# Kernel optimization log

Hardware: AMD Instinct MI355X
Metric: run time of the kernel (lower is better)

## Reference

```python
import jax, jax.numpy as jnp
import numpy as np

N = 100000   # nodes
E = 1600000  # edges
DIN, H, DOUT = 128, 64, 40
EPS = 1e-5

def setup_inputs() -> dict:
    key = jax.random.key(0)
    ks = jax.random.split(key, 8)
    def w(k, fan_in, shape):
        return jax.random.normal(k, shape, jnp.float32) * (1.0 / np.sqrt(fan_in))
    return {
        "node_feat": jax.random.normal(ks[0], (N, DIN), jnp.float32),
        "edge_index": jax.random.randint(ks[1], (2, E), 0, N, dtype=jnp.int32),
        "W1": w(ks[2], DIN, (DIN, H)), "b1": jnp.zeros((H,), jnp.float32),
        "g1": jnp.ones((H,), jnp.float32), "beta1": jnp.zeros((H,), jnp.float32),
        "W2": w(ks[3], H, (H, H)), "b2": jnp.zeros((H,), jnp.float32),
        "g2": jnp.ones((H,), jnp.float32), "beta2": jnp.zeros((H,), jnp.float32),
        "W3": w(ks[4], H, (H, H)), "b3": jnp.zeros((H,), jnp.float32),
        "Wf": w(ks[5], H, (H, DOUT)), "bf": jnp.zeros((DOUT,), jnp.float32),
    }

def _gcn_conv(x, src, dst, norm, W, b):
    # x: [N, Cin] -> linear then D^{-1/2}(A+I)D^{-1/2} aggregation (PyG GCNConv)
    h = x @ W                              # [N, Cout]
    msg = h[src] * norm[:, None]           # [E+N, Cout] gather + scale
    return jax.ops.segment_sum(msg, dst, num_segments=N) + b

def _bn(x, g, b):
    # BatchNorm1d over node dim with batch statistics (biased var)
    m = jnp.mean(x, axis=0)
    v = jnp.mean((x - m) ** 2, axis=0)
    return (x - m) * jax.lax.rsqrt(v + EPS) * g + b

def reference(node_feat, edge_index, W1, b1, g1, beta1, W2, b2, g2, beta2, W3, b3, Wf, bf):
    loop = jnp.arange(N, dtype=edge_index.dtype)
    src = jnp.concatenate([edge_index[0], loop])   # add self loops
    dst = jnp.concatenate([edge_index[1], loop])
    deg = jax.ops.segment_sum(jnp.ones_like(src, dtype=node_feat.dtype), dst, num_segments=N)
    dis = jax.lax.rsqrt(deg)                        # deg >= 1 (self loops)
    norm = dis[src] * dis[dst]                      # [E+N]

    x1 = jax.nn.relu(_bn(_gcn_conv(node_feat, src, dst, norm, W1, b1), g1, beta1))
    # dropout is identity in eval mode
    x2 = jax.nn.relu(_bn(_gcn_conv(x1, src, dst, norm, W2, b2), g2, beta2))
    x3 = _gcn_conv(x2, src, dst, norm, W3, b3)

    x = jnp.max(jnp.stack([x1, x2, x3], axis=0), axis=0)  # JumpingKnowledge 'max'
    return x @ Wf + bf
```

## Files before the change

### kernel.cpp

```cpp
#include <hip/hip_runtime.h>

#define NN 100000
#define NE 1600000
#define DIN 128
#define HDIM 64
#define DOUT 40
#define EPS 1e-5f
#define NXCD 8
#define CAP 64

typedef int int4v __attribute__((ext_vector_type(4)));
typedef float f4v __attribute__((ext_vector_type(4)));

__device__ __forceinline__ float bf2f(unsigned short v) {
    return __uint_as_float(((unsigned int)v) << 16);
}
__device__ __forceinline__ unsigned short f2bf(float f) {
    unsigned int u = __float_as_uint(f);
    u += 0x7FFFu + ((u >> 16) & 1u);
    return (unsigned short)(u >> 16);
}

__device__ __forceinline__ int ntl(const int* p) { return __builtin_nontemporal_load(p); }
__device__ __forceinline__ int4v ntl4(const int4v* p) { return __builtin_nontemporal_load(p); }
__device__ __forceinline__ f4v ntlf4(const f4v* p) { return __builtin_nontemporal_load(p); }

__global__ __launch_bounds__(256) void fill_kernel(const int* __restrict__ ei,
                                                   int* __restrict__ cnt,
                                                   int* __restrict__ esrc) {
    const int xcd = blockIdx.x & (NXCD - 1);
    const int lo = xcd * (NN / NXCD);
    const int hi = (xcd == NXCD - 1) ? NN : lo + (NN / NXCD);
    const int slot = blockIdx.x >> 3;
    const int nslot = gridDim.x >> 3;
    const int4v* d4 = (const int4v*)(ei + NE);
    for (int e4 = slot * blockDim.x + threadIdx.x; e4 < NE / 4; e4 += nslot * blockDim.x) {
        int4v d = ntl4(d4 + e4);
#pragma unroll
        for (int k = 0; k < 4; ++k) {
            int dd = d[k];
            if (dd >= lo && dd < hi) {
                int pos = atomicAdd(&cnt[dd], 1);
                if (pos < CAP) {
                    esrc[(dd << 6) + pos] = ntl(ei + 4 * e4 + k);
                }
            }
        }
    }
}

__global__ __launch_bounds__(256) void dis_kernel(const int* __restrict__ cnt,
                                                  float* __restrict__ dis) {
    for (int i = blockIdx.x * blockDim.x + threadIdx.x; i < NN; i += gridDim.x * blockDim.x)
        dis[i] = rsqrtf((float)(cnt[i] + 1));
}

template <int K, int TR, bool BN, bool NTL>
__global__ __launch_bounds__(256) void gemm_lds(const float* __restrict__ x,
                                                const float* __restrict__ W,
                                                const float* __restrict__ dis,
                                                const float* __restrict__ sc,
                                                const float* __restrict__ sh,
                                                unsigned short* __restrict__ h2) {
    __shared__ float xs[TR][K];
    const int tid = threadIdx.x;
    const int lane = tid & 63;
    const int wv = tid >> 6;
    float w[K];
#pragma unroll
    for (int k = 0; k < K; ++k) w[k] = W[k * 64 + lane];

    float4 scv, shv;
    if (BN) {
        const int c4 = tid & (K / 4 - 1);
        scv = ((const float4*)sc)[c4];
        shv = ((const float4*)sh)[c4];
    }

    const int row0 = blockIdx.x * TR;
    const int remRows = NN - row0;
    const int nvec = ((remRows >= TR) ? TR : remRows) * K / 4;
    const f4v* srcv = (const f4v*)(x + (long long)row0 * K);
    f4v* dstv = (f4v*)&xs[0][0];
    for (int i = tid; i < nvec; i += 256) {
        f4v v = NTL ? ntlf4(srcv + i) : srcv[i];
        if (BN) {
            v.x = fmaxf(fmaf(v.x, scv.x, shv.x), 0.f);
            v.y = fmaxf(fmaf(v.y, scv.y, shv.y), 0.f);
            v.z = fmaxf(fmaf(v.z, scv.z, shv.z), 0.f);
            v.w = fmaxf(fmaf(v.w, scv.w, shv.w), 0.f);
        }
        dstv[i] = v;
    }
    __syncthreads();

    const int rpw = TR / 4;
#pragma unroll
    for (int rr = 0; rr < rpw; ++rr) {
        const int r = wv * rpw + rr;
        const int row = row0 + r;
        if (row >= NN) break;
        float a0 = 0.f, a1 = 0.f, a2 = 0.f, a3 = 0.f;
#pragma unroll
        for (int k = 0; k < K; k += 4) {
            float4 xv = *(const float4*)&xs[r][k];
            a0 = fmaf(xv.x, w[k + 0], a0);
            a1 = fmaf(xv.y, w[k + 1], a1);
            a2 = fmaf(xv.z, w[k + 2], a2);
            a3 = fmaf(xv.w, w[k + 3], a3);
        }
        h2[row * 64 + lane] = f2bf(((a0 + a1) + (a2 + a3)) * dis[row]);
    }
}

__global__ __launch_bounds__(256) void agg_csr(const int* __restrict__ cnt,
                                               const int* __restrict__ esrc,
                                               const float* __restrict__ dis,
                                               const unsigned short* __restrict__ h2,
                                               float* __restrict__ y) {
    const int tid = threadIdx.x;
    const int wv = tid >> 6;
    const int lane = tid & 63;
    const int half = lane >> 5;
    const int c = lane & 31;
    const int node = blockIdx.x * 8 + wv * 2 + half;
    const ushort2* h2v = (const ushort2*)h2;
    ushort2 p0 = h2v[node * 32 + c];
    float ax = bf2f(p0.x), ay = bf2f(p0.y);
    const int deg = min(cnt[node], CAP);
    const int m = max(deg, __shfl_xor(deg, 32));
    const int jb = node << 6;
#pragma unroll 8
    for (int t = 0; t < m; ++t) {
        int sv = esrc[jb + t];
        int s = (t < deg) ? sv : NN;
        ushort2 p = h2v[s * 32 + c];
        ax += bf2f(p.x);
        ay += bf2f(p.y);
    }
    float dn = dis[node];
    ((float2*)(y + node * 64))[c] = make_float2(ax * dn, ay * dn);
}

__global__ __launch_bounds__(256) void agg_final(const int* __restrict__ cnt,
                                                 const int* __restrict__ esrc,
                                                 const float* __restrict__ dis,
                                                 const unsigned short* __restrict__ h2,
                                                 const float* __restrict__ x1,
                                                 const float* __restrict__ x2,
                                                 const float* __restrict__ sc1,
                                                 const float* __restrict__ sh1,
                                                 const float* __restrict__ sc2,
                                                 const float* __restrict__ sh2,
                                                 const float* __restrict__ b3,
                                                 const float* __restrict__ Wf,
                                                 const float* __restrict__ bf,
                                                 float* __restrict__ out) {
    __shared__ float m[8][64];
    const int tid = threadIdx.x;
    const int wv = tid >> 6;
    const int lane = tid & 63;
    const int half = lane >> 5;
    const int c = lane & 31;
    const int node = blockIdx.x * 8 + wv * 2 + half;
    const ushort2* h2v = (const ushort2*)h2;
    ushort2 p0 = h2v[node * 32 + c];
    float ax = bf2f(p0.x), ay = bf2f(p0.y);
    const int deg = min(cnt[node], CAP);
    const int mm = max(deg, __shfl_xor(deg, 32));
    const int jb = node << 6;
#pragma unroll 8
    for (int t = 0; t < mm; ++t) {
        int sv = esrc[jb + t];
        int s = (t < deg) ? sv : NN;
        ushort2 p = h2v[s * 32 + c];
        ax += bf2f(p.x);
        ay += bf2f(p.y);
    }
    const float dn = dis[node];
    const int c0 = 2 * c;
    const int o = node * 64 + c0;
    float2 x1v = *(const float2*)(x1 + o);
    float2 x2v = *(const float2*)(x2 + o);
    float v3x = fmaf(ax, dn, b3[c0]);
    float v3y = fmaf(ay, dn, b3[c0 + 1]);
    float v1x = fmaxf(fmaf(x1v.x, sc1[c0], sh1[c0]), 0.f);
    float v1y = fmaxf(fmaf(x1v.y, sc1[c0 + 1], sh1[c0 + 1]), 0.f);
    float v2x = fmaxf(fmaf(x2v.x, sc2[c0], sh2[c0]), 0.f);
    float v2y = fmaxf(fmaf(x2v.y, sc2[c0 + 1], sh2[c0 + 1]), 0.f);
    const int rl = wv * 2 + half;
    m[rl][c0] = fmaxf(fmaxf(v1x, v2x), v3x);
    m[rl][c0 + 1] = fmaxf(fmaxf(v1y, v2y), v3y);
    __syncthreads();
#pragma unroll
    for (int rr = wv; rr < 8; rr += 4) {
        if (lane < DOUT) {
            float a2 = bf[lane];
#pragma unroll
            for (int k = 0; k < 64; ++k) a2 += m[rr][k] * Wf[k * DOUT + lane];
            out[(blockIdx.x * 8 + rr) * DOUT + lane] = a2;
        }
    }
}

__global__ __launch_bounds__(256) void stats_kernel(const float* __restrict__ y, float* stats) {
    const int tid = threadIdx.x;
    const int c = tid & 63, rg = tid >> 6;
    float s = 0.f, s2 = 0.f;
    for (int row = blockIdx.x * 4 + rg; row < NN; row += gridDim.x * 4) {
        float v = y[row * 64 + c];
        s += v;
        s2 += v * v;
    }
    __shared__ float ls[256], ls2[256];
    ls[tid] = s; ls2[tid] = s2;
    __syncthreads();
    if (tid < 64) {
        s = ls[tid] + ls[tid + 64] + ls[tid + 128] + ls[tid + 192];
        s2 = ls2[tid] + ls2[tid + 64] + ls2[tid + 128] + ls2[tid + 192];
        atomicAdd(&stats[tid], s);
        atomicAdd(&stats[64 + tid], s2);
    }
}

__global__ __launch_bounds__(64) void bn_coef(const float* __restrict__ stats,
                                              const float* __restrict__ g,
                                              const float* __restrict__ beta,
                                              float* __restrict__ sc,
                                              float* __restrict__ sh) {
    const int c = threadIdx.x;
    const float invN = 1.0f / NN;
    float m = stats[c] * invN;
    float var = stats[64 + c] * invN - m * m;
    float s = g[c] * rsqrtf(var + EPS);
    sc[c] = s;
    sh[c] = beta[c] - m * s;
}

extern "C" void kernel_launch(void* const* d_in, const int* in_sizes, int n_in,
                              void* d_out, int out_size, void* d_ws, size_t ws_size,
                              hipStream_t stream) {
    const float* node_feat = (const float*)d_in[0];
    const int*   ei        = (const int*)d_in[1];
    const float* W1 = (const float*)d_in[2];
    const float* g1 = (const float*)d_in[4];
    const float* beta1 = (const float*)d_in[5];
    const float* W2 = (const float*)d_in[6];
    const float* g2 = (const float*)d_in[8];
    const float* beta2 = (const float*)d_in[9];
    const float* W3 = (const float*)d_in[10];
    const float* b3 = (const float*)d_in[11];
    const float* Wf = (const float*)d_in[12];
    const float* bf = (const float*)d_in[13];
    float* out = (float*)d_out;

    float* ws  = (float*)d_ws;
    float* dis = ws;
    unsigned short* h2 = (unsigned short*)(dis + NN);
    float* x1  = (float*)(h2 + (NN + 1) * 64);
    float* x2  = x1 + NN * 64;
    float* stats = x2 + NN * 64;
    float* sc1 = stats + 128;
    float* sh1 = sc1 + 64;
    float* sc2 = sh1 + 64;
    float* sh2 = sc2 + 64;
    int* cnt  = (int*)(sh2 + 64);
    int* esrc = cnt + NN;

    const int B = 256;
    const int gElem = 2048;
    const int gAgg = NN / 8;

    hipMemsetAsync(cnt, 0, NN * sizeof(int), stream);
    hipMemsetAsync(h2 + NN * 64, 0, 64 * sizeof(unsigned short), stream);
    fill_kernel<<<gElem, B, 0, stream>>>(ei, cnt, esrc);
    dis_kernel<<<512, B, 0, stream>>>(cnt, dis);

    gemm_lds<DIN, 32, false, true><<<(NN + 31) / 32, B, 0, stream>>>(node_feat, W1, dis, nullptr, nullptr, h2);
    agg_csr<<<gAgg, B, 0, stream>>>(cnt, esrc, dis, h2, x1);
    hipMemsetAsync(stats, 0, 128 * sizeof(float), stream);
    stats_kernel<<<512, B, 0, stream>>>(x1, stats);
    bn_coef<<<1, 64, 0, stream>>>(stats, g1, beta1, sc1, sh1);

    gemm_lds<HDIM, 64, true, false><<<(NN + 63) / 64, B, 0, stream>>>(x1, W2, dis, sc1, sh1, h2);
    agg_csr<<<gAgg, B, 0, stream>>>(cnt, esrc, dis, h2, x2);
    hipMemsetAsync(stats, 0, 128 * sizeof(float), stream);
    stats_kernel<<<512, B, 0, stream>>>(x2, stats);
    bn_coef<<<1, 64, 0, stream>>>(stats, g2, beta2, sc2, sh2);

    gemm_lds<HDIM, 64, true, false><<<(NN + 63) / 64, B, 0, stream>>>(x2, W3, dis, sc2, sh2, h2);
    agg_final<<<gAgg, B, 0, stream>>>(cnt, esrc, dis, h2, x1, x2,
                                      sc1, sh1, sc2, sh2, b3, Wf, bf, out);
}
```

Before: 407.1 us.

## Fuse BN statistics into aggregation and store hidden activations as bf16

The aggregation kernel now writes its output as bf16 and also emits per-block partial sums and sums of squares. A small reduce kernel combines those partials, replacing the separate statistics pass that reread the full fp32 activations. The hidden-layer GEMMs and the final kernel read bf16 activations, which halves that traffic. The cost is extra bf16 rounding on x1/x2 before BN and in the jumping-knowledge max, and the BN statistics are taken from the unrounded fp32 values while the normalisation is applied to the rounded ones.

After: 381.2 us. 6.4% less time.

```diff
diff --git a/kernel.cpp b/kernel.cpp
--- a/kernel.cpp
+++ b/kernel.cpp
@@ -8,9 +8,11 @@
 #define EPS 1e-5f
 #define NXCD 8
 #define CAP 64
+#define NAGG (NN / 8)
 
 typedef int int4v __attribute__((ext_vector_type(4)));
 typedef float f4v __attribute__((ext_vector_type(4)));
+typedef unsigned short u16x8 __attribute__((ext_vector_type(8)));
 
 __device__ __forceinline__ float bf2f(unsigned short v) {
     return __uint_as_float(((unsigned int)v) << 16);
@@ -55,43 +57,24 @@
         dis[i] = rsqrtf((float)(cnt[i] + 1));
 }
 
-template <int K, int TR, bool BN, bool NTL>
-__global__ __launch_bounds__(256) void gemm_lds(const float* __restrict__ x,
+__global__ __launch_bounds__(256) void gemm_f32(const float* __restrict__ x,
                                                 const float* __restrict__ W,
                                                 const float* __restrict__ dis,
-                                                const float* __restrict__ sc,
-                                                const float* __restrict__ sh,
                                                 unsigned short* __restrict__ h2) {
-    __shared__ float xs[TR][K];
+    const int K = DIN, TR = 32;
+    __shared__ float xs[TR][DIN];
     const int tid = threadIdx.x;
     const int lane = tid & 63;
     const int wv = tid >> 6;
-    float w[K];
+    float w[DIN];
 #pragma unroll
     for (int k = 0; k < K; ++k) w[k] = W[k * 64 + lane];
 
-    float4 scv, shv;
-    if (BN) {
-        const int c4 = tid & (K / 4 - 1);
-        scv = ((const float4*)sc)[c4];
-        shv = ((const float4*)sh)[c4];
-    }
-
     const int row0 = blockIdx.x * TR;
-    const int remRows = NN - row0;
-    const int nvec = ((remRows >= TR) ? TR : remRows) * K / 4;
+    const int nvec = TR * K / 4;
     const f4v* srcv = (const f4v*)(x + (long long)row0 * K);
     f4v* dstv = (f4v*)&xs[0][0];
-    for (int i = tid; i < nvec; i += 256) {
-        f4v v = NTL ? ntlf4(srcv + i) : srcv[i];
-        if (BN) {
-            v.x = fmaxf(fmaf(v.x, scv.x, shv.x), 0.f);
-            v.y = fmaxf(fmaf(v.y, scv.y, shv.y), 0.f);
-            v.z = fmaxf(fmaf(v.z, scv.z, shv.z), 0.f);
-            v.w = fmaxf(fmaf(v.w, scv.w, shv.w), 0.f);
-        }
-        dstv[i] = v;
-    }
+    for (int i = tid; i < nvec; i += 256) dstv[i] = ntlf4(srcv + i);
     __syncthreads();
 
     const int rpw = TR / 4;
@@ -99,7 +82,6 @@
     for (int rr = 0; rr < rpw; ++rr) {
         const int r = wv * rpw + rr;
         const int row = row0 + r;
-        if (row >= NN) break;
         float a0 = 0.f, a1 = 0.f, a2 = 0.f, a3 = 0.f;
 #pragma unroll
         for (int k = 0; k < K; k += 4) {
@@ -113,11 +95,68 @@
     }
 }
 
+template <int TR>
+__global__ __launch_bounds__(256) void gemm_bf16(const unsigned short* __restrict__ x16,
+                                                 const float* __restrict__ W,
+                                                 const float* __restrict__ dis,
+                                                 const float* __restrict__ sc,
+                                                 const float* __restrict__ sh,
+                                                 unsigned short* __restrict__ h2) {
+    __shared__ float xs[TR][HDIM];
+    const int tid = threadIdx.x;
+    const int lane = tid & 63;
+    const int wv = tid >> 6;
+    float w[HDIM];
+#pragma unroll
+    for (int k = 0; k < HDIM; ++k) w[k] = W[k * 64 + lane];
+
+    const int cg = tid & 7;
+    float scl[8], shl[8];
+#pragma unroll
+    for (int j = 0; j < 8; ++j) { scl[j] = sc[cg * 8 + j]; shl[j] = sh[cg * 8 + j]; }
+
+    const int row0 = blockIdx.x * TR;
+    const int remRows = NN - row0;
+    const int nvec = ((remRows >= TR) ? TR : remRows) * 8;
+    const u16x8* srcv = (const u16x8*)(x16 + (long long)row0 * 64);
+    for (int i = tid; i < nvec; i += 256) {
+        u16x8 v = srcv[i];
+        float f[8];
+#pragma unroll
+        for (int j = 0; j < 8; ++j)
+            f[j] = fmaxf(fmaf(bf2f(v[j]), scl[j], shl[j]), 0.f);
+        float* dst = &xs[0][0] + i * 8;
+        ((f4v*)dst)[0] = *(f4v*)&f[0];
+        ((f4v*)dst)[1] = *(f4v*)&f[4];
+    }
+    __syncthreads();
+
+    const int rpw = TR / 4;
+#pragma unroll
+    for (int rr = 0; rr < rpw; ++rr) {
+        const int r = wv * rpw + rr;
+        const int row = row0 + r;
+        if (row >= NN) break;
+        float a0 = 0.f, a1 = 0.f, a2 = 0.f, a3 = 0.f;
+#pragma unroll
+        for (int k = 0; k < HDIM; k += 4) {
+            float4 xv = *(const float4*)&xs[r][k];
+            a0 = fmaf(xv.x, w[k + 0], a0);
+            a1 = fmaf(xv.y, w[k + 1], a1);
+            a2 = fmaf(xv.z, w[k + 2], a2);
+            a3 = fmaf(xv.w, w[k + 3], a3);
+        }
+        h2[row * 64 + lane] = f2bf(((a0 + a1) + (a2 + a3)) * dis[row]);
+    }
+}
+
 __global__ __launch_bounds__(256) void agg_csr(const int* __restrict__ cnt,
                                                const int* __restrict__ esrc,
                                                const float* __restrict__ dis,
                                                const unsigned short* __restrict__ h2,
-                                               float* __restrict__ y) {
+                                               unsigned short* __restrict__ y16,
+                                               float* __restrict__ part) {
+    __shared__ float sm[8][64];
     const int tid = threadIdx.x;
     const int wv = tid >> 6;
     const int lane = tid & 63;
@@ -138,16 +177,56 @@
         ax += bf2f(p.x);
         ay += bf2f(p.y);
     }
-    float dn = dis[node];
-    ((float2*)(y + node * 64))[c] = make_float2(ax * dn, ay * dn);
+    const float dn = dis[node];
+    ax *= dn; ay *= dn;
+    ushort2 o; o.x = f2bf(ax); o.y = f2bf(ay);
+    ((ushort2*)y16)[node * 32 + c] = o;
+    const int rl = wv * 2 + half;
+    sm[rl][2 * c] = ax;
+    sm[rl][2 * c + 1] = ay;
+    __syncthreads();
+    if (tid < 64) {
+        float s = 0.f, s2 = 0.f;
+#pragma unroll
+        for (int r = 0; r < 8; ++r) {
+            float v = sm[r][tid];
+            s += v;
+            s2 = fmaf(v, v, s2);
+        }
+        part[blockIdx.x * 128 + tid] = s;
+        part[blockIdx.x * 128 + 64 + tid] = s2;
+    }
+}
+
+__global__ __launch_bounds__(128) void stats_reduce(const float* __restrict__ part,
+                                                    float* __restrict__ stats) {
+    const int tid = threadIdx.x;
+    const int r0 = blockIdx.x * (NAGG / 100);
+    float s = 0.f;
+    for (int r = r0; r < r0 + NAGG / 100; ++r) s += part[r * 128 + tid];
+    atomicAdd(&stats[tid], s);
+}
+
+__global__ __launch_bounds__(64) void bn_coef(const float* __restrict__ stats,
+                                              const float* __restrict__ g,
+                                              const float* __restrict__ beta,
+                                              float* __restrict__ sc,
+                                              float* __restrict__ sh) {
+    const int c = threadIdx.x;
+    const float invN = 1.0f / NN;
+    float m = stats[c] * invN;
+    float var = stats[64 + c] * invN - m * m;
+    float s = g[c] * rsqrtf(var + EPS);
+    sc[c] = s;
+    sh[c] = beta[c] - m * s;
 }
 
 __global__ __launch_bounds__(256) void agg_final(const int* __restrict__ cnt,
                                                  const int* __restrict__ esrc,
                                                  const float* __restrict__ dis,
                                                  const unsigned short* __restrict__ h2,
-                                                 const float* __restrict__ x1,
-                                                 const float* __restrict__ x2,
+                                                 const unsigned short* __restrict__ x1,
+                                                 const unsigned short* __restrict__ x2,
                                                  const float* __restrict__ sc1,
                                                  const float* __restrict__ sh1,
                                                  const float* __restrict__ sc2,
@@ -179,15 +258,14 @@
     }
     const float dn = dis[node];
     const int c0 = 2 * c;
-    const int o = node * 64 + c0;
-    float2 x1v = *(const float2*)(x1 + o);
-    float2 x2v = *(const float2*)(x2 + o);
+    ushort2 x1u = ((const ushort2*)x1)[node * 32 + c];
+    ushort2 x2u = ((const ushort2*)x2)[node * 32 + c];
     float v3x = fmaf(ax, dn, b3[c0]);
     float v3y = fmaf(ay, dn, b3[c0 + 1]);
-    float v1x = fmaxf(fmaf(x1v.x, sc1[c0], sh1[c0]), 0.f);
-    float v1y = fmaxf(fmaf(x1v.y, sc1[c0 + 1], sh1[c0 + 1]), 0.f);
-    float v2x = fmaxf(fmaf(x2v.x, sc2[c0], sh2[c0]), 0.f);
-    float v2y = fmaxf(fmaf(x2v.y, sc2[c0 + 1], sh2[c0 + 1]), 0.f);
+    float v1x = fmaxf(fmaf(bf2f(x1u.x), sc1[c0], sh1[c0]), 0.f);
+    float v1y = fmaxf(fmaf(bf2f(x1u.y), sc1[c0 + 1], sh1[c0 + 1]), 0.f);
+    float v2x = fmaxf(fmaf(bf2f(x2u.x), sc2[c0], sh2[c0]), 0.f);
+    float v2y = fmaxf(fmaf(bf2f(x2u.y), sc2[c0 + 1], sh2[c0 + 1]), 0.f);
     const int rl = wv * 2 + half;
     m[rl][c0] = fmaxf(fmaxf(v1x, v2x), v3x);
     m[rl][c0 + 1] = fmaxf(fmaxf(v1y, v2y), v3y);
@@ -201,40 +279,6 @@
             out[(blockIdx.x * 8 + rr) * DOUT + lane] = a2;
         }
     }
-}
-
-__global__ __launch_bounds__(256) void stats_kernel(const float* __restrict__ y, float* stats) {
-    const int tid = threadIdx.x;
-    const int c = tid & 63, rg = tid >> 6;
-    float s = 0.f, s2 = 0.f;
-    for (int row = blockIdx.x * 4 + rg; row < NN; row += gridDim.x * 4) {
-        float v = y[row * 64 + c];
-        s += v;
-        s2 += v * v;
-    }
-    __shared__ float ls[256], ls2[256];
-    ls[tid] = s; ls2[tid] = s2;
-    __syncthreads();
-    if (tid < 64) {
-        s = ls[tid] + ls[tid + 64] + ls[tid + 128] + ls[tid + 192];
-        s2 = ls2[tid] + ls2[tid + 64] + ls2[tid + 128] + ls2[tid + 192];
-        atomicAdd(&stats[tid], s);
-        atomicAdd(&stats[64 + tid], s2);
-    }
-}
-
-__global__ __launch_bounds__(64) void bn_coef(const float* __restrict__ stats,
-                                              const float* __restrict__ g,
-                                              const float* __restrict__ beta,
-                                              float* __restrict__ sc,
-                                              float* __restrict__ sh) {
-    const int c = threadIdx.x;
-    const float invN = 1.0f / NN;
-    float m = stats[c] * invN;
-    float var = stats[64 + c] * invN - m * m;
-    float s = g[c] * rsqrtf(var + EPS);
-    sc[c] = s;
-    sh[c] = beta[c] - m * s;
 }
 
 extern "C" void kernel_launch(void* const* d_in, const int* in_sizes, int n_in,
@@ -257,9 +301,10 @@
     float* ws  = (float*)d_ws;
     float* dis = ws;
     unsigned short* h2 = (unsigned short*)(dis + NN);
-    float* x1  = (float*)(h2 + (NN + 1) * 64);
-    float* x2  = x1 + NN * 64;
-    float* stats = x2 + NN * 64;
+    unsigned short* x1 = h2 + (NN + 1) * 64;
+    unsigned short* x2 = x1 + NN * 64;
+    float* part = (float*)(x2 + NN * 64);
+    float* stats = part + NAGG * 128;
     float* sc1 = stats + 128;
     float* sh1 = sc1 + 64;
     float* sc2 = sh1 + 64;
@@ -269,26 +314,26 @@
 
     const int B = 256;
     const int gElem = 2048;
-    const int gAgg = NN / 8;
+    const int gAgg = NAGG;
 
     hipMemsetAsync(cnt, 0, NN * sizeof(int), stream);
     hipMemsetAsync(h2 + NN * 64, 0, 64 * sizeof(unsigned short), stream);
     fill_kernel<<<gElem, B, 0, stream>>>(ei, cnt, esrc);
     dis_kernel<<<512, B, 0, stream>>>(cnt, dis);
 
-    gemm_lds<DIN, 32, false, true><<<(NN + 31) / 32, B, 0, stream>>>(node_feat, W1, dis, nullptr, nullptr, h2);
-    agg_csr<<<gAgg, B, 0, stream>>>(cnt, esrc, dis, h2, x1);
+    gemm_f32<<<NN / 32, B, 0, stream>>>(node_feat, W1, dis, h2);
+    agg_csr<<<gAgg, B, 0, stream>>>(cnt, esrc, dis, h2, x1, part);
     hipMemsetAsync(stats, 0, 128 * sizeof(float), stream);
-    stats_kernel<<<512, B, 0, stream>>>(x1, stats);
+    stats_reduce<<<100, 128, 0, stream>>>(part, stats);
     bn_coef<<<1, 64, 0, stream>>>(stats, g1, beta1, sc1, sh1);
 
-    gemm_lds<HDIM, 64, true, false><<<(NN + 63) / 64, B, 0, stream>>>(x1, W2, dis, sc1, sh1, h2);
-    agg_csr<<<gAgg, B, 0, stream>>>(cnt, esrc, dis, h2, x2);
+    gemm_bf16<64><<<(NN + 63) / 64, B, 0, stream>>>(x1, W2, dis, sc1, sh1, h2);
+    agg_csr<<<gAgg, B, 0, stream>>>(cnt, esrc, dis, h2, x2, part);
     hipMemsetAsync(stats, 0, 128 * sizeof(float), stream);
-    stats_kernel<<<512, B, 0, stream>>>(x2, stats);
+    stats_reduce<<<100, 128, 0, stream>>>(part, stats);
     bn_coef<<<1, 64, 0, stream>>>(stats, g2, beta2, sc2, sh2);
 
-    gemm_lds<HDIM, 64, true, false><<<(NN + 63) / 64, B, 0, stream>>>(x2, W3, dis, sc2, sh2, h2);
+    gemm_bf16<64><<<(NN + 63) / 64, B, 0, stream>>>(x2, W3, dis, sc2, sh2, h2);
     agg_final<<<gAgg, B, 0, stream>>>(cnt, esrc, dis, h2, x1, x2,
                                       sc1, sh1, sc2, sh2, b3, Wf, bf, out);
 }
```
